# Kernel tuning notes

Hardware: AMD Instinct MI355X
Metric: run time of the kernel (lower is better)

## Reference

```python
import jax, jax.numpy as jnp
import numpy as np
from jax import lax

PROP_TIME = 18
K_F = 3
NUM = K_F * K_F - 1   # 8 non-center taps
IDX_REF = NUM // 2    # 4


def _bilinear(img, ys, xs):
    """img: (H,W). ys/xs: (T,H,W) absolute coords. Zero padding outside."""
    H, W = img.shape
    y0 = jnp.floor(ys)
    x0 = jnp.floor(xs)
    wy = ys - y0
    wx = xs - x0
    y0i = y0.astype(jnp.int32)
    x0i = x0.astype(jnp.int32)

    def g(yi, xi):
        valid = (yi >= 0) & (yi < H) & (xi >= 0) & (xi < W)
        v = img[jnp.clip(yi, 0, H - 1), jnp.clip(xi, 0, W - 1)]
        return jnp.where(valid, v, 0.0)

    v00 = g(y0i, x0i)
    v01 = g(y0i, x0i + 1)
    v10 = g(y0i + 1, x0i)
    v11 = g(y0i + 1, x0i + 1)
    return (v00 * (1 - wy) * (1 - wx) + v01 * (1 - wy) * wx
            + v10 * wy * (1 - wx) + v11 * wy * wx)


_sample_b = jax.vmap(_bilinear, in_axes=(0, 0, 0))  # batched over B


def setup_inputs() -> dict:
    key = jax.random.key(0)
    k1, k2, k3, k4, k5 = jax.random.split(key, 5)
    B, H, W = 4, 480, 640
    CH_G = 8
    return {
        "feat_init": jax.random.uniform(k1, (B, 1, H, W), dtype=jnp.float32),
        "guidance": jax.random.normal(k2, (B, CH_G, H, W), dtype=jnp.float32),
        "confidence": jax.random.uniform(k3, (B, 1, H, W), dtype=jnp.float32),
        "w_oa": jax.random.normal(k4, (3 * NUM, CH_G, 3, 3), dtype=jnp.float32) * 0.1,
        "b_oa": jax.random.normal(k5, (3 * NUM,), dtype=jnp.float32) * 0.01,
        "aff_scale_const": jnp.ones((1,), jnp.float32) * (0.5 * NUM),  # gamma*num (TGASS)
    }


def reference(feat_init, guidance, confidence, w_oa, b_oa, aff_scale_const):
    B, _, H, W = guidance.shape

    # offset / affinity head: Conv2d(ch_g, 3*num, k=3, pad=1)
    oa = lax.conv_general_dilated(
        guidance, w_oa, window_strides=(1, 1), padding=((1, 1), (1, 1)),
        dimension_numbers=("NCHW", "OIHW", "NCHW")) + b_oa[None, :, None, None]
    o1, o2, aff = jnp.split(oa, 3, axis=1)  # each (B, 8, H, W): dy, dx, raw aff

    # insert zero offset for the center (reference) tap -> 9 taps
    z = jnp.zeros((B, 1, H, W), o1.dtype)
    off_y = jnp.concatenate([o1[:, :IDX_REF], z, o1[:, IDX_REF:]], axis=1)  # (B,9,H,W)
    off_x = jnp.concatenate([o2[:, :IDX_REF], z, o2[:, IDX_REF:]], axis=1)

    # TGASS affinity
    aff = jnp.tanh(aff) / (aff_scale_const + 1e-8)

    # confidence propagation: 1x1 deform conv per non-center tap with w_conf=1,
    # modulation=1 -> bilinear sample of confidence at p + offset (offset detached)
    nc = jnp.array([0, 1, 2, 3, 5, 6, 7, 8])
    base_y = jnp.arange(H, dtype=jnp.float32)[:, None]
    base_x = jnp.arange(W, dtype=jnp.float32)[None, :]
    yc = base_y[None, None] + lax.stop_gradient(off_y[:, nc])  # (B,8,H,W)
    xc = base_x[None, None] + lax.stop_gradient(off_x[:, nc])
    conf_aff = _sample_b(confidence[:, 0], yc, xc)             # (B,8,H,W)
    aff = aff * conf_aff

    # absolute-sum normalization (TGASS: clamp denom at 1)
    s = jnp.sum(jnp.abs(aff), axis=1, keepdims=True) + 1e-4
    s = jnp.maximum(s, 1.0)
    aff = aff / s
    aff_ref = 1.0 - jnp.sum(aff, axis=1, keepdims=True)
    aff9 = jnp.concatenate([aff[:, :IDX_REF], aff_ref, aff[:, IDX_REF:]], axis=1)
    aff9 = jax.nn.softmax(aff9, axis=1)  # (B,9,H,W)

    # propagation sampling coords: p + kernel_tap + learned offset (fixed per iter)
    kh = jnp.repeat(jnp.arange(-1, 2, dtype=jnp.float32), 3)  # (9,)
    kw = jnp.tile(jnp.arange(-1, 2, dtype=jnp.float32), 3)
    ys = base_y[None, None] + kh[None, :, None, None] + off_y  # (B,9,H,W)
    xs = base_x[None, None] + kw[None, :, None, None] + off_x

    def step(feat, _):
        samp = _sample_b(feat[:, 0], ys, xs)                  # (B,9,H,W)
        new = jnp.sum(aff9 * samp, axis=1, keepdims=True)     # (B,1,H,W)
        return new, None

    feat_result, _ = lax.scan(step, feat_init, None, length=PROP_TIME)
    return feat_result
```

## Files before the change

kernel.cpp:

```cpp
#include <hip/hip_runtime.h>
#include <hip/hip_fp16.h>
#include <math.h>

#define BB 4
#define HH 480
#define WW 640
#define HW (HH * WW)
#define PP (BB * HW)

__device__ __forceinline__ float ldz(const float* __restrict__ img, int y, int x) {
    bool v = ((unsigned)y < (unsigned)HH) & ((unsigned)x < (unsigned)WW);
    int off = v ? (y * WW + x) : 0;
    float val = img[off];
    return v ? val : 0.0f;
}

__device__ __forceinline__ void axis_map(int y0, float wy, int H,
                                         int& c0, float& t, float& s) {
    if (y0 >= 0 && y0 <= H - 2)      { c0 = y0;    t = wy;   s = 1.0f; }
    else if (y0 == -1)               { c0 = 0;     t = 0.0f; s = wy; }
    else if (y0 == H - 1)            { c0 = H - 2; t = 1.0f; s = 1.0f - wy; }
    else                             { c0 = 0;     t = 0.0f; s = 0.0f; }
}

__global__ void transpose_w_kernel(const float* __restrict__ w_oa, float* __restrict__ wT) {
    for (int i = threadIdx.x; i < 1728; i += 256) {
        const int k = i / 192;
        const int r = i - k * 192;
        const int ci = r / 24;
        const int c = r - ci * 24;
        wT[i] = w_oa[c * 72 + ci * 9 + k];
    }
}

__global__ __launch_bounds__(256) void precompute_kernel(
    const float* __restrict__ guidance,
    const float* __restrict__ confidence,
    const float* __restrict__ wT,
    const float* __restrict__ b_oa,
    const float* __restrict__ aff_scale,
    uint4* __restrict__ PK4,
    float* __restrict__ affC)
{
    const int p = blockIdx.x * 256 + threadIdx.x;
    const int b = p / HW;
    const int rem = p - b * HW;
    const int y = rem / WW;
    const int x = rem - y * WW;

    float acc[24];
    #pragma unroll
    for (int c = 0; c < 24; ++c) acc[c] = b_oa[c];

    const float* gb = guidance + (size_t)b * 8 * HW;

    #pragma unroll 1
    for (int kidx = 0; kidx < 9; ++kidx) {
        const int yy = y + kidx / 3 - 1;
        const int xx = x + kidx % 3 - 1;
        const bool valid = ((unsigned)yy < (unsigned)HH) & ((unsigned)xx < (unsigned)WW);
        const int base = valid ? (yy * WW + xx) : 0;
        float g[8];
        #pragma unroll
        for (int ci = 0; ci < 8; ++ci) {
            float v = gb[ci * HW + base];
            g[ci] = valid ? v : 0.0f;
        }
        const float* wk = wT + kidx * 192;
        #pragma unroll
        for (int ci = 0; ci < 8; ++ci) {
            const float gv = g[ci];
            #pragma unroll
            for (int c = 0; c < 24; ++c)
                acc[c] = fmaf(gv, wk[ci * 24 + c], acc[c]);
        }
    }

    const float inv_scale = 1.0f / (aff_scale[0] + 1e-8f);
    const float* cb = confidence + (size_t)b * HW;
    const float fy = (float)y, fx = (float)x;

    float affv[8];
    #pragma unroll
    for (int j = 0; j < 8; ++j) {
        const float oy = acc[j], ox = acc[8 + j];
        const float a = tanhf(acc[16 + j]) * inv_scale;
        const float ysj = fy + oy, xsj = fx + ox;
        const float y0f = floorf(ysj), x0f = floorf(xsj);
        const float wy = ysj - y0f, wx = xsj - x0f;
        const int y0 = (int)y0f, x0 = (int)x0f;
        const float v00 = ldz(cb, y0, x0),     v01 = ldz(cb, y0, x0 + 1);
        const float v10 = ldz(cb, y0 + 1, x0), v11 = ldz(cb, y0 + 1, x0 + 1);
        const float conf = v00 * (1.0f - wy) * (1.0f - wx) + v01 * (1.0f - wy) * wx
                         + v10 * wy * (1.0f - wx)          + v11 * wy * wx;
        affv[j] = a * conf;
    }

    float s = 1e-4f;
    #pragma unroll
    for (int j = 0; j < 8; ++j) s += fabsf(affv[j]);
    s = fmaxf(s, 1.0f);
    const float inv_s = 1.0f / s;
    float sum = 0.0f;
    #pragma unroll
    for (int j = 0; j < 8; ++j) { affv[j] *= inv_s; sum += affv[j]; }
    const float aref = 1.0f - sum;

    float m = aref;
    #pragma unroll
    for (int j = 0; j < 8; ++j) m = fmaxf(m, affv[j]);
    float e[8];
    float denom = 0.0f;
    #pragma unroll
    for (int j = 0; j < 8; ++j) { e[j] = expf(affv[j] - m); denom += e[j]; }
    denom += expf(aref - m);
    const float invden = 1.0f / denom;

    affC[p] = expf(aref - m) * invden * 8192.0f;

    unsigned ba[8], tt[8];
    #pragma unroll
    for (int j = 0; j < 8; ++j) {
        const int t9 = (j < 4) ? j : j + 1;
        const float khv = (float)(t9 / 3 - 1);
        const float kwv = (float)(t9 % 3 - 1);
        const float ys = (fy + khv) + acc[j];
        const float xs = (fx + kwv) + acc[8 + j];
        const float y0f = floorf(ys), x0f = floorf(xs);
        const float wy = ys - y0f, wx = xs - x0f;
        int y0c, x0c; float ty, tx, sy, sx;
        axis_map((int)y0f, wy, HH, y0c, ty, sy);
        axis_map((int)x0f, wx, WW, x0c, tx, sx);

        const float aeff = (e[j] * invden) * sy * sx;
        unsigned aq = __float2uint_rn(aeff * 8192.0f);
        aq = aq > 8191u ? 8191u : aq;
        ba[j] = ((unsigned)(y0c * WW + x0c) << 13) | aq;
        __half2 h2 = __floats2half2_rn(ty, tx);
        tt[j] = __builtin_bit_cast(unsigned, h2);
    }
    PK4[4 * p + 0] = make_uint4(ba[0], tt[0], ba[1], tt[1]);
    PK4[4 * p + 1] = make_uint4(ba[2], tt[2], ba[3], tt[3]);
    PK4[4 * p + 2] = make_uint4(ba[4], tt[4], ba[5], tt[5]);
    PK4[4 * p + 3] = make_uint4(ba[6], tt[6], ba[7], tt[7]);
}

__global__ __launch_bounds__(256) void prop_kernel(
    const float* __restrict__ src,
    float* __restrict__ dst,
    const uint4* __restrict__ PK4,
    const float* __restrict__ affC)
{
    const int p = blockIdx.x * 256 + threadIdx.x;
    const int b = p / HW;
    const float* fb = src + (size_t)b * HW;

    const uint4 q0 = PK4[4 * p + 0];
    const uint4 q1 = PK4[4 * p + 1];
    const uint4 q2 = PK4[4 * p + 2];
    const uint4 q3 = PK4[4 * p + 3];

    float acc = 0.0f;

    auto tap = [&](unsigned bav, unsigned tw) {
        const float af = (float)(bav & 8191u);
        const float* g = fb + (bav >> 13);
        const float2 top2 = *reinterpret_cast<const float2*>(g);
        const float2 bot2 = *reinterpret_cast<const float2*>(g + WW);
        const float2 t = __half22float2(__builtin_bit_cast(__half2, tw));
        const float top = fmaf(t.y, top2.y - top2.x, top2.x);
        const float bot = fmaf(t.y, bot2.y - bot2.x, bot2.x);
        acc = fmaf(af, fmaf(t.x, bot - top, top), acc);
    };
    tap(q0.x, q0.y); tap(q0.z, q0.w);
    tap(q1.x, q1.y); tap(q1.z, q1.w);
    tap(q2.x, q2.y); tap(q2.z, q2.w);
    tap(q3.x, q3.y); tap(q3.z, q3.w);

    dst[p] = fmaf(affC[p], src[p], acc) * (1.0f / 8192.0f);
}

extern "C" void kernel_launch(void* const* d_in, const int* in_sizes, int n_in,
                              void* d_out, int out_size, void* d_ws, size_t ws_size,
                              hipStream_t stream) {
    const float* feat_init  = (const float*)d_in[0];
    const float* guidance   = (const float*)d_in[1];
    const float* confidence = (const float*)d_in[2];
    const float* w_oa       = (const float*)d_in[3];
    const float* b_oa       = (const float*)d_in[4];
    const float* aff_scale  = (const float*)d_in[5];
    float* out = (float*)d_out;
    float* ws  = (float*)d_ws;

    const size_t need = (size_t)18 * PP * sizeof(float);
    if (ws_size < need) return;

    uint4* PK4  = reinterpret_cast<uint4*>(ws);
    float* affC = ws + (size_t)16 * PP;
    float* bufA = ws + (size_t)17 * PP;
    float* wT   = bufA;

    const int grid = PP / 256;
    transpose_w_kernel<<<1, 256, 0, stream>>>(w_oa, wT);
    precompute_kernel<<<grid, 256, 0, stream>>>(guidance, confidence, wT, b_oa,
                                                aff_scale, PK4, affC);

    const float* src = feat_init;
    for (int i = 0; i < 18; ++i) {
        float* dst = (i & 1) ? out : bufA;
        prop_kernel<<<grid, 256, 0, stream>>>(src, dst, PK4, affC);
        src = dst;
    }
}
```

Measured before the change: 562.5 us.

## Stage feature halo tile in shared memory for propagation gathers

The propagation kernel now maps each block to a 64x4 pixel tile and loads a 12x80 halo of the source feature into LDS. Bilinear taps whose coordinates fall inside the halo read from LDS, and the rest fall back to global loads. The packed index is re-encoded as separate y/x fields so taps can be range-checked. The precompute kernel also swaps tanhf/expf for fast __expf-based approximations, which may slightly change the quantized weights. Out-of-halo taps diverge and the LDS fill and sync add latency per iteration.

```diff
diff --git a/kernel.cpp b/kernel.cpp
--- a/kernel.cpp
+++ b/kernel.cpp
@@ -7,6 +7,12 @@
 #define WW 640
 #define HW (HH * WW)
 #define PP (BB * HW)
+
+#define TW 64
+#define TH 4
+#define CWID 80
+#define RHGT 12
+#define TPB (HH/TH * WW/TW)
 
 __device__ __forceinline__ float ldz(const float* __restrict__ img, int y, int x) {
     bool v = ((unsigned)y < (unsigned)HH) & ((unsigned)x < (unsigned)WW);
@@ -21,6 +27,10 @@
     else if (y0 == -1)               { c0 = 0;     t = 0.0f; s = wy; }
     else if (y0 == H - 1)            { c0 = H - 2; t = 1.0f; s = 1.0f - wy; }
     else                             { c0 = 0;     t = 0.0f; s = 0.0f; }
+}
+
+__device__ __forceinline__ float tanh_fast(float x) {
+    return 1.0f - 2.0f / (__expf(2.0f * x) + 1.0f);
 }
 
 __global__ void transpose_w_kernel(const float* __restrict__ w_oa, float* __restrict__ wT) {
@@ -84,7 +94,7 @@
     #pragma unroll
     for (int j = 0; j < 8; ++j) {
         const float oy = acc[j], ox = acc[8 + j];
-        const float a = tanhf(acc[16 + j]) * inv_scale;
+        const float a = tanh_fast(acc[16 + j]) * inv_scale;
         const float ysj = fy + oy, xsj = fx + ox;
         const float y0f = floorf(ysj), x0f = floorf(xsj);
         const float wy = ysj - y0f, wx = xsj - x0f;
@@ -112,11 +122,12 @@
     float e[8];
     float denom = 0.0f;
     #pragma unroll
-    for (int j = 0; j < 8; ++j) { e[j] = expf(affv[j] - m); denom += e[j]; }
-    denom += expf(aref - m);
+    for (int j = 0; j < 8; ++j) { e[j] = __expf(affv[j] - m); denom += e[j]; }
+    const float ec = __expf(aref - m);
+    denom += ec;
     const float invden = 1.0f / denom;
 
-    affC[p] = expf(aref - m) * invden * 8192.0f;
+    affC[p] = ec * invden * 8192.0f;
 
     unsigned ba[8], tt[8];
     #pragma unroll
@@ -135,7 +146,7 @@
         const float aeff = (e[j] * invden) * sy * sx;
         unsigned aq = __float2uint_rn(aeff * 8192.0f);
         aq = aq > 8191u ? 8191u : aq;
-        ba[j] = ((unsigned)(y0c * WW + x0c) << 13) | aq;
+        ba[j] = ((((unsigned)y0c << 10) | (unsigned)x0c) << 13) | aq;
         __half2 h2 = __floats2half2_rn(ty, tx);
         tt[j] = __builtin_bit_cast(unsigned, h2);
     }
@@ -151,25 +162,65 @@
     const uint4* __restrict__ PK4,
     const float* __restrict__ affC)
 {
-    const int p = blockIdx.x * 256 + threadIdx.x;
-    const int b = p / HW;
+    __shared__ float tile[RHGT * CWID];
+
+    const int tid = threadIdx.x;
+    const int blk = blockIdx.x;
+    const int b = blk / TPB;
+    const int r = blk - b * TPB;
+    const int ty0 = (r / (WW / TW)) * TH;
+    const int tx0 = (r - (r / (WW / TW)) * (WW / TW)) * TW;
+    const int ry0 = ty0 - 4;
+    const int cx0 = tx0 - 8;
+
     const float* fb = src + (size_t)b * HW;
+
+    #pragma unroll
+    for (int i = 0; i < 4; ++i) {
+        const int idx = tid + i * 256;
+        if (idx < RHGT * CWID) {
+            const int rr = idx / CWID;
+            const int cc = idx - rr * CWID;
+            const int gy = ry0 + rr, gx = cx0 + cc;
+            if (((unsigned)gy < (unsigned)HH) & ((unsigned)gx < (unsigned)WW))
+                tile[idx] = fb[gy * WW + gx];
+        }
+    }
+    __syncthreads();
+
+    const int lx = tid & 63, ly = tid >> 6;
+    const int y = ty0 + ly, x = tx0 + lx;
+    const int p = b * HW + y * WW + x;
 
     const uint4 q0 = PK4[4 * p + 0];
     const uint4 q1 = PK4[4 * p + 1];
     const uint4 q2 = PK4[4 * p + 2];
     const uint4 q3 = PK4[4 * p + 3];
 
-    float acc = 0.0f;
+    float acc = affC[p] * tile[(ly + 4) * CWID + lx + 8];
+
+    const int base_off = ry0 * CWID + cx0;
 
     auto tap = [&](unsigned bav, unsigned tw) {
         const float af = (float)(bav & 8191u);
-        const float* g = fb + (bav >> 13);
-        const float2 top2 = *reinterpret_cast<const float2*>(g);
-        const float2 bot2 = *reinterpret_cast<const float2*>(g + WW);
+        const int y0c = (int)(bav >> 23);
+        const int x0c = (int)((bav >> 13) & 1023u);
+        float v00, v01, v10, v11;
+        const bool in = ((unsigned)(y0c - ry0) < (unsigned)(RHGT - 1)) &
+                        ((unsigned)(x0c - cx0) < (unsigned)(CWID - 1));
+        if (__builtin_expect(in, 1)) {
+            const int l = y0c * CWID + x0c - base_off;
+            v00 = tile[l];          v01 = tile[l + 1];
+            v10 = tile[l + CWID];   v11 = tile[l + CWID + 1];
+        } else {
+            const float* g = fb + (y0c * WW + x0c);
+            const float2 t2 = *reinterpret_cast<const float2*>(g);
+            const float2 b2 = *reinterpret_cast<const float2*>(g + WW);
+            v00 = t2.x; v01 = t2.y; v10 = b2.x; v11 = b2.y;
+        }
         const float2 t = __half22float2(__builtin_bit_cast(__half2, tw));
-        const float top = fmaf(t.y, top2.y - top2.x, top2.x);
-        const float bot = fmaf(t.y, bot2.y - bot2.x, bot2.x);
+        const float top = fmaf(t.y, v01 - v00, v00);
+        const float bot = fmaf(t.y, v11 - v10, v10);
         acc = fmaf(af, fmaf(t.x, bot - top, top), acc);
     };
     tap(q0.x, q0.y); tap(q0.z, q0.w);
@@ -177,7 +228,7 @@
     tap(q2.x, q2.y); tap(q2.z, q2.w);
     tap(q3.x, q3.y); tap(q3.z, q3.w);
 
-    dst[p] = fmaf(affC[p], src[p], acc) * (1.0f / 8192.0f);
+    dst[p] = acc * (1.0f / 8192.0f);
 }
 
 extern "C" void kernel_launch(void* const* d_in, const int* in_sizes, int n_in,
@@ -205,10 +256,10 @@
     precompute_kernel<<<grid, 256, 0, stream>>>(guidance, confidence, wT, b_oa,
                                                 aff_scale, PK4, affC);
 
-    const float* src = feat_init;
+    const float* srcp = feat_init;
     for (int i = 0; i < 18; ++i) {
-        float* dst = (i & 1) ? out : bufA;
-        prop_kernel<<<grid, 256, 0, stream>>>(src, dst, PK4, affC);
-        src = dst;
-    }
-}
+        float* dstp = (i & 1) ? out : bufA;
+        prop_kernel<<<grid, 256, 0, stream>>>(srcp, dstp, PK4, affC);
+        srcp = dstp;
+    }
+}
```

New measurement: 563.2 us. Within noise of the previous version (+0.1%).
